# Kernel tuning notes

Hardware: AMD Instinct MI355X
Metric: run time of the kernel (lower is better)

## Reference

```python
import jax, jax.numpy as jnp
import numpy as np

MARGIN = 1.0  # cur_margin for LBA_inverted_loss=True
COS_SCALE = 128.0


def smoothed_metric_loss(X, margin=MARGIN):
    # X: [B, E]. Lifted structured loss with inverted cosine similarity.
    B = X.shape[0]
    P = B // 2
    D = (X @ X.T) / COS_SCALE            # [B, B]
    E = jnp.exp(margin + D)              # [B, B]
    # For pair p (rows i=2p, j=2p+1): sum E over rows {i,j}, all columns except {i,j}.
    Eb = E.reshape(P, 2, P, 2)           # [P, 2, P, 2]
    row_sums = Eb.sum(axis=(1, 2, 3))    # [P] full sum over both rows of pair p
    idx = jnp.arange(P)
    diag_block = Eb[idx, :, idx, :].sum(axis=(1, 2))  # [P] the excluded 2x2 block
    S = row_sums - diag_block            # [P] masked sums
    Dij = D.reshape(P, 2, P, 2)[idx, 0, idx, 1]       # [P] D[i, j]
    J = jnp.log(S) - Dij
    return 0.5 * jnp.mean(J * J)


def reference(text_embeddings, shape_embeddings):
    B = text_embeddings.shape[0]
    # shape_embeddings repeated twice per model: row k -> shape[k // 2]
    shape_rep = jnp.repeat(shape_embeddings, 2, axis=0)      # [B, E]
    metric_tt = smoothed_metric_loss(text_embeddings)
    # mask rows: even rows keep text, odd rows take repeated shape embedding
    even = (jnp.arange(B) % 2 == 0)[:, None]
    mixed = jnp.where(even, text_embeddings, shape_rep)      # [B, E]
    metric_st = smoothed_metric_loss(mixed)
    return metric_tt + metric_st


def setup_inputs() -> dict:
    key = jax.random.key(0)
    k1, k2 = jax.random.split(key)
    B, E = 8192, 128
    text_embeddings = jax.random.normal(k1, (B, E), dtype=jnp.float32)
    shape_embeddings = jax.random.normal(k2, (B // 2, E), dtype=jnp.float32)
    return {"text_embeddings": text_embeddings, "shape_embeddings": shape_embeddings}
```

## Files before the change

kernel.cpp:

```cpp
#include <hip/hip_runtime.h>
#include <hip/hip_bf16.h>


#define B_ROWS 8192
#define E_COLS 128
#define P_PAIRS 4096
#define NSTRIP 128
#define NH 8

using f32x4 = __attribute__((ext_vector_type(4))) float;
using i32x8 = __attribute__((ext_vector_type(8))) int;

#define BF_SCALE 0.106164482742544f
#define EULER    2.718281828459045f
#define SCALE1   0x7f

__device__ __forceinline__ unsigned pk4_fp8(float a, float b, float c, float d) {
    unsigned v = 0;
    v = __builtin_amdgcn_cvt_pk_fp8_f32(a * BF_SCALE, b * BF_SCALE, v, false);
    v = __builtin_amdgcn_cvt_pk_fp8_f32(c * BF_SCALE, d * BF_SCALE, v, true);
    return v;
}

__device__ __forceinline__ int lds_off(int row, int k0) {
    return (row << 7) + (k0 ^ ((row & 7) << 4));
}

__device__ __forceinline__ i32x8 load_frag32(const char* base, int row, int k32) {
    union { i32x8 v; int4 h[2]; } u;
    u.h[0] = *(const int4*)(base + lds_off(row, k32));
    u.h[1] = *(const int4*)(base + lds_off(row, k32 + 16));
    return u.v;
}

__device__ __forceinline__ void stage8k(const char* gsrc, char* ldst, int tid) {
#pragma unroll
    for (int it = 0; it < 2; ++it) {
        int L   = it * 4096 + tid * 16;
        int row = L >> 7;
        int cb  = L & 127;
        int src = (row << 7) + (cb ^ ((row & 7) << 4));
        __builtin_amdgcn_global_load_lds(
            (const __attribute__((address_space(1))) void*)(gsrc + src),
            (__attribute__((address_space(3))) void*)(ldst + L), 16, 0, 0);
    }
}

__global__ void convert_kernel(const float* __restrict__ text,
                               const float* __restrict__ shape,
                               unsigned* __restrict__ Xt,
                               unsigned* __restrict__ Xm,
                               float* __restrict__ R,
                               float* __restrict__ out) {
    int idx = blockIdx.x * blockDim.x + threadIdx.x;
    if (idx >= B_ROWS * E_COLS / 4) return;
    if (idx < 4096) {
        float4 z; z.x = z.y = z.z = z.w = 0.f;
        ((float4*)R)[idx] = z;
    }
    if (idx == 0) *out = 0.f;
    int e = idx * 4;
    float4 t = *(const float4*)(text + e);
    unsigned tp = pk4_fp8(t.x, t.y, t.z, t.w);
    Xt[idx] = tp;
    int row = e >> 7;
    if (row & 1) {
        int col = e & 127;
        float4 s = *(const float4*)(shape + (row >> 1) * E_COLS + col);
        Xm[idx] = pk4_fp8(s.x, s.y, s.z, s.w);
    } else {
        Xm[idx] = tp;
    }
}

__launch_bounds__(256, 8)
__global__ void gemm_rowsum_kernel(const unsigned char* __restrict__ Xt,
                                   const unsigned char* __restrict__ Xm,
                                   float* __restrict__ R) {
    const int bm = blockIdx.x, h = blockIdx.y, l = blockIdx.z;
    const char* gX = (const char*)(l ? Xm : Xt);

    __shared__ __align__(16) char buf0[64 * 128];
    __shared__ __align__(16) char buf1[64 * 128];
    const int tid = threadIdx.x;

    const int t0 = (h == 0) ? NH : h;
    const int N  = (h == 0) ? (bm < 64 ? 8 : 7) : 8;

    stage8k(gX + (size_t)bm * 8192, buf0, tid);
    stage8k(gX + (size_t)((bm + t0) & 127) * 8192, buf1, tid);
    asm volatile("s_waitcnt vmcnt(2)" ::: "memory");
    __builtin_amdgcn_s_barrier();

    const int lane = tid & 63;
    const int w  = tid >> 6;
    const int wr = w >> 1, wc = w & 1;
    const int rA0 = wr * 32 + (lane & 15);
    const int rB0 = wc * 32 + (lane & 15);
    const int k32 = (lane >> 4) * 32;

    i32x8 afr[2];
#pragma unroll
    for (int m = 0; m < 2; ++m)
        afr[m] = load_frag32(buf0, rA0 + m * 16, k32);

    float s_r[2][4] = {{0.f}};

    if (h == 0) {
        i32x8 bfr[2];
#pragma unroll
        for (int n = 0; n < 2; ++n)
            bfr[n] = load_frag32(buf0, rB0 + n * 16, k32);
        f32x4 acc[2][2] = {};
#pragma unroll
        for (int m = 0; m < 2; ++m)
#pragma unroll
            for (int n = 0; n < 2; ++n)
                acc[m][n] = __builtin_amdgcn_mfma_scale_f32_16x16x128_f8f6f4(
                    afr[m], bfr[n], acc[m][n], 0, 0, 0, SCALE1, 0, SCALE1);
#pragma unroll
        for (int m = 0; m < 2; ++m)
#pragma unroll
            for (int n = 0; n < 2; ++n)
#pragma unroll
                for (int j = 0; j < 4; ++j)
                    s_r[m][j] += __builtin_amdgcn_exp2f(acc[m][n][j]);
    }

    asm volatile("s_waitcnt lgkmcnt(0)" ::: "memory");
    __builtin_amdgcn_s_barrier();

    int cur = 1;
    for (int idx = 0; idx < N; ++idx) {
        const bool hasnext = (idx + 1 < N);
        if (hasnext)
            stage8k(gX + (size_t)((bm + t0 + NH * (idx + 1)) & 127) * 8192,
                    cur ? buf0 : buf1, tid);

        if (hasnext) { asm volatile("s_waitcnt vmcnt(2)" ::: "memory"); }
        else         { asm volatile("s_waitcnt vmcnt(0)" ::: "memory"); }
        __builtin_amdgcn_s_barrier();

        const char* lsrc = cur ? buf1 : buf0;
        i32x8 bfr[2];
#pragma unroll
        for (int n = 0; n < 2; ++n)
            bfr[n] = load_frag32(lsrc, rB0 + n * 16, k32);
        f32x4 acc[2][2] = {};
#pragma unroll
        for (int m = 0; m < 2; ++m)
#pragma unroll
            for (int n = 0; n < 2; ++n)
                acc[m][n] = __builtin_amdgcn_mfma_scale_f32_16x16x128_f8f6f4(
                    afr[m], bfr[n], acc[m][n], 0, 0, 0, SCALE1, 0, SCALE1);

        asm volatile("s_waitcnt lgkmcnt(0)" ::: "memory");
        __builtin_amdgcn_s_barrier();

        const int bn = (bm + t0 + NH * idx) & 127;
        float s_c[2] = {0.f, 0.f};
#pragma unroll
        for (int m = 0; m < 2; ++m)
#pragma unroll
            for (int n = 0; n < 2; ++n)
#pragma unroll
                for (int j = 0; j < 4; ++j) {
                    float e2 = __builtin_amdgcn_exp2f(acc[m][n][j]);
                    s_r[m][j] += e2;
                    s_c[n] += e2;
                }
#pragma unroll
        for (int n = 0; n < 2; ++n) {
            float v = s_c[n];
            v += __shfl_xor(v, 16, 64);
            v += __shfl_xor(v, 32, 64);
            if (lane < 16) {
                int gcol = bn * 64 + wc * 32 + n * 16 + lane;
                atomicAdd(&R[l * B_ROWS + gcol], EULER * v);
            }
        }
        cur ^= 1;
    }

#pragma unroll
    for (int m = 0; m < 2; ++m)
#pragma unroll
        for (int j = 0; j < 4; ++j) {
            float v = s_r[m][j];
            v += __shfl_xor(v, 1, 64);
            v += __shfl_xor(v, 2, 64);
            v += __shfl_xor(v, 4, 64);
            v += __shfl_xor(v, 8, 64);
            if ((lane & 15) == 0) {
                int grow = bm * 64 + wr * 32 + m * 16 + (lane >> 4) * 4 + j;
                atomicAdd(&R[l * B_ROWS + grow], EULER * v);
            }
        }
}

__global__ void finalize_kernel(const float* __restrict__ text,
                                const float* __restrict__ shape,
                                const float* __restrict__ R,
                                float* __restrict__ out) {
    const int tid = threadIdx.x;
    const int lane = tid & 63;
    const int w = tid >> 6;
    const float inv128 = 0.0078125f;
    float accum = 0.f;

    for (int task = blockIdx.x * 4 + w; task < 2 * P_PAIRS; task += 1024) {
        int l = task >> 12;
        int p = task & (P_PAIRS - 1);
        const float* a = text + (2 * p) * E_COLS;
        const float* b = l ? (shape + p * E_COLS) : (text + (2 * p + 1) * E_COLS);
        float2 av = *(const float2*)(a + lane * 2);
        float2 bv = *(const float2*)(b + lane * 2);
        float dii = av.x * av.x + av.y * av.y;
        float djj = bv.x * bv.x + bv.y * bv.y;
        float dij = av.x * bv.x + av.y * bv.y;
#pragma unroll
        for (int sh = 1; sh < 64; sh <<= 1) {
            dii += __shfl_xor(dii, sh, 64);
            djj += __shfl_xor(djj, sh, 64);
            dij += __shfl_xor(dij, sh, 64);
        }
        if (lane == 0) {
            float Dii = dii * inv128, Djj = djj * inv128, Dij = dij * inv128;
            float S = R[l * B_ROWS + 2 * p] + R[l * B_ROWS + 2 * p + 1]
                    - (__expf(1.f + Dii) + 2.f * __expf(1.f + Dij) + __expf(1.f + Djj));
            float J = __logf(S) - Dij;
            accum += 0.5f * J * J * (1.0f / (float)P_PAIRS);
        }
    }

    __shared__ float red[4];
    if (lane == 0) red[w] = accum;
    __syncthreads();
    if (tid == 0) atomicAdd(out, red[0] + red[1] + red[2] + red[3]);
}

extern "C" void kernel_launch(void* const* d_in, const int* in_sizes, int n_in,
                              void* d_out, int out_size, void* d_ws, size_t ws_size,
                              hipStream_t stream) {
    const float* text  = (const float*)d_in[0];
    const float* shape = (const float*)d_in[1];
    float* out = (float*)d_out;
    char* ws = (char*)d_ws;

    unsigned char* Xt = (unsigned char*)ws;
    unsigned char* Xm = (unsigned char*)(ws + 1u * 1024u * 1024u);
    float* R = (float*)(ws + 2u * 1024u * 1024u);

    convert_kernel<<<(B_ROWS * E_COLS / 4 + 255) / 256, 256, 0, stream>>>(
        text, shape, (unsigned*)Xt, (unsigned*)Xm, R, out);

    dim3 grid(NSTRIP, NH, 2);
    gemm_rowsum_kernel<<<grid, 256, 0, stream>>>(Xt, Xm, R);

    finalize_kernel<<<256, 256, 0, stream>>>(text, shape, R, out);
}
```

Baseline: 48.25 us.

## Restructure GEMM tile per-wave with private triple-buffered LDS and no barriers

Each wave now owns all 64 A rows (loaded directly from global into registers) and a private 16-row slice of B, staged into its own triple-buffered LDS region. This removes the block-wide barriers and shared double buffer. The loop is fully unrolled over 8 tiles, and the h==0 case's extra tile is masked by multiplying by zero instead of running a variable trip count. MFMA sections get raised priority, and launch bounds drop to 5 blocks per SM to make room for the larger register footprint. The masked tile still spends its exp and atomic work.

```diff
diff --git a/kernel.cpp b/kernel.cpp
--- a/kernel.cpp
+++ b/kernel.cpp
@@ -22,28 +22,11 @@
     return v;
 }
 
-__device__ __forceinline__ int lds_off(int row, int k0) {
-    return (row << 7) + (k0 ^ ((row & 7) << 4));
-}
-
-__device__ __forceinline__ i32x8 load_frag32(const char* base, int row, int k32) {
+__device__ __forceinline__ i32x8 load_frag32_g(const char* rowbase, int k32) {
     union { i32x8 v; int4 h[2]; } u;
-    u.h[0] = *(const int4*)(base + lds_off(row, k32));
-    u.h[1] = *(const int4*)(base + lds_off(row, k32 + 16));
+    u.h[0] = *(const int4*)(rowbase + k32);
+    u.h[1] = *(const int4*)(rowbase + k32 + 16);
     return u.v;
-}
-
-__device__ __forceinline__ void stage8k(const char* gsrc, char* ldst, int tid) {
-#pragma unroll
-    for (int it = 0; it < 2; ++it) {
-        int L   = it * 4096 + tid * 16;
-        int row = L >> 7;
-        int cb  = L & 127;
-        int src = (row << 7) + (cb ^ ((row & 7) << 4));
-        __builtin_amdgcn_global_load_lds(
-            (const __attribute__((address_space(1))) void*)(gsrc + src),
-            (__attribute__((address_space(3))) void*)(ldst + L), 16, 0, 0);
-    }
 }
 
 __global__ void convert_kernel(const float* __restrict__ text,
@@ -73,117 +56,113 @@
     }
 }
 
-__launch_bounds__(256, 8)
+__launch_bounds__(256, 5)
 __global__ void gemm_rowsum_kernel(const unsigned char* __restrict__ Xt,
                                    const unsigned char* __restrict__ Xm,
                                    float* __restrict__ R) {
     const int bm = blockIdx.x, h = blockIdx.y, l = blockIdx.z;
     const char* gX = (const char*)(l ? Xm : Xt);
 
-    __shared__ __align__(16) char buf0[64 * 128];
-    __shared__ __align__(16) char buf1[64 * 128];
-    const int tid = threadIdx.x;
+    __shared__ __align__(16) char lds[4][3][16 * 128];
+    const int tid  = threadIdx.x;
+    const int lane = tid & 63;
+    const int w    = tid >> 6;
 
     const int t0 = (h == 0) ? NH : h;
-    const int N  = (h == 0) ? (bm < 64 ? 8 : 7) : 8;
-
-    stage8k(gX + (size_t)bm * 8192, buf0, tid);
-    stage8k(gX + (size_t)((bm + t0) & 127) * 8192, buf1, tid);
-    asm volatile("s_waitcnt vmcnt(2)" ::: "memory");
-    __builtin_amdgcn_s_barrier();
-
-    const int lane = tid & 63;
-    const int w  = tid >> 6;
-    const int wr = w >> 1, wc = w & 1;
-    const int rA0 = wr * 32 + (lane & 15);
-    const int rB0 = wc * 32 + (lane & 15);
-    const int k32 = (lane >> 4) * 32;
-
-    i32x8 afr[2];
-#pragma unroll
-    for (int m = 0; m < 2; ++m)
-        afr[m] = load_frag32(buf0, rA0 + m * 16, k32);
-
-    float s_r[2][4] = {{0.f}};
+    const float g7 = (h == 0 && bm >= 64) ? 0.f : 1.f;
+
+    const int lrow = lane & 15;
+    const int kb   = (lane >> 4) * 32;
+
+    auto stage = [&](int bn, char* dst) {
+        const char* base = gX + (size_t)bn * 8192 + w * (16 * 128);
+#pragma unroll
+        for (int it = 0; it < 2; ++it) {
+            int sr  = it * 8 + (lane >> 3);
+            int cb  = (lane & 7) * 16;
+            int src = sr * 128 + (cb ^ ((sr & 7) << 4));
+            __builtin_amdgcn_global_load_lds(
+                (const __attribute__((address_space(1))) void*)(base + src),
+                (__attribute__((address_space(3))) void*)(dst + it * 1024), 16, 0, 0);
+        }
+    };
+    auto ldfrag = [&](const char* regn) {
+        union { i32x8 v; int4 h2[2]; } u;
+        u.h2[0] = *(const int4*)(regn + lrow * 128 + (kb        ^ ((lrow & 7) << 4)));
+        u.h2[1] = *(const int4*)(regn + lrow * 128 + ((kb + 16) ^ ((lrow & 7) << 4)));
+        return u.v;
+    };
+    auto bn_of = [&](int k) { return (bm + t0 + 8 * k) & 127; };
+
+    const char* Ag = gX + (size_t)bm * 8192;
+    i32x8 afr[4];
+#pragma unroll
+    for (int m = 0; m < 4; ++m)
+        afr[m] = load_frag32_g(Ag + (size_t)(m * 16 + lrow) * 128, kb);
+
+    i32x8 db = {};
+    if (h == 0)
+        db = load_frag32_g(Ag + (size_t)(w * 16 + lrow) * 128, kb);
+
+    stage(bn_of(0), &lds[w][0][0]);
+    stage(bn_of(1), &lds[w][1][0]);
+
+    asm volatile("s_waitcnt vmcnt(4)" ::: "memory");
+
+    float s_r[4][4] = {{0.f}};
 
     if (h == 0) {
-        i32x8 bfr[2];
-#pragma unroll
-        for (int n = 0; n < 2; ++n)
-            bfr[n] = load_frag32(buf0, rB0 + n * 16, k32);
-        f32x4 acc[2][2] = {};
-#pragma unroll
-        for (int m = 0; m < 2; ++m)
-#pragma unroll
-            for (int n = 0; n < 2; ++n)
-                acc[m][n] = __builtin_amdgcn_mfma_scale_f32_16x16x128_f8f6f4(
-                    afr[m], bfr[n], acc[m][n], 0, 0, 0, SCALE1, 0, SCALE1);
-#pragma unroll
-        for (int m = 0; m < 2; ++m)
-#pragma unroll
-            for (int n = 0; n < 2; ++n)
-#pragma unroll
-                for (int j = 0; j < 4; ++j)
-                    s_r[m][j] += __builtin_amdgcn_exp2f(acc[m][n][j]);
-    }
-
-    asm volatile("s_waitcnt lgkmcnt(0)" ::: "memory");
-    __builtin_amdgcn_s_barrier();
-
-    int cur = 1;
-    for (int idx = 0; idx < N; ++idx) {
-        const bool hasnext = (idx + 1 < N);
-        if (hasnext)
-            stage8k(gX + (size_t)((bm + t0 + NH * (idx + 1)) & 127) * 8192,
-                    cur ? buf0 : buf1, tid);
-
-        if (hasnext) { asm volatile("s_waitcnt vmcnt(2)" ::: "memory"); }
-        else         { asm volatile("s_waitcnt vmcnt(0)" ::: "memory"); }
-        __builtin_amdgcn_s_barrier();
-
-        const char* lsrc = cur ? buf1 : buf0;
-        i32x8 bfr[2];
-#pragma unroll
-        for (int n = 0; n < 2; ++n)
-            bfr[n] = load_frag32(lsrc, rB0 + n * 16, k32);
-        f32x4 acc[2][2] = {};
-#pragma unroll
-        for (int m = 0; m < 2; ++m)
-#pragma unroll
-            for (int n = 0; n < 2; ++n)
-                acc[m][n] = __builtin_amdgcn_mfma_scale_f32_16x16x128_f8f6f4(
-                    afr[m], bfr[n], acc[m][n], 0, 0, 0, SCALE1, 0, SCALE1);
-
-        asm volatile("s_waitcnt lgkmcnt(0)" ::: "memory");
-        __builtin_amdgcn_s_barrier();
-
-        const int bn = (bm + t0 + NH * idx) & 127;
-        float s_c[2] = {0.f, 0.f};
-#pragma unroll
-        for (int m = 0; m < 2; ++m)
-#pragma unroll
-            for (int n = 0; n < 2; ++n)
-#pragma unroll
-                for (int j = 0; j < 4; ++j) {
-                    float e2 = __builtin_amdgcn_exp2f(acc[m][n][j]);
-                    s_r[m][j] += e2;
-                    s_c[n] += e2;
-                }
-#pragma unroll
-        for (int n = 0; n < 2; ++n) {
-            float v = s_c[n];
-            v += __shfl_xor(v, 16, 64);
-            v += __shfl_xor(v, 32, 64);
-            if (lane < 16) {
-                int gcol = bn * 64 + wc * 32 + n * 16 + lane;
-                atomicAdd(&R[l * B_ROWS + gcol], EULER * v);
+        f32x4 acc[4] = {};
+#pragma unroll
+        for (int m = 0; m < 4; ++m)
+            acc[m] = __builtin_amdgcn_mfma_scale_f32_16x16x128_f8f6f4(
+                afr[m], db, acc[m], 0, 0, 0, SCALE1, 0, SCALE1);
+#pragma unroll
+        for (int m = 0; m < 4; ++m)
+#pragma unroll
+            for (int j = 0; j < 4; ++j)
+                s_r[m][j] += __builtin_amdgcn_exp2f(acc[m][j]);
+    }
+
+#pragma unroll
+    for (int k = 0; k < 8; ++k) {
+        if (k + 2 < 8)
+            stage(bn_of(k + 2), &lds[w][(k + 2) % 3][0]);
+
+        if (k + 2 < 8)      { asm volatile("s_waitcnt vmcnt(4)" ::: "memory"); }
+        else if (k + 1 < 8) { asm volatile("s_waitcnt vmcnt(2)" ::: "memory"); }
+        else                { asm volatile("s_waitcnt vmcnt(0)" ::: "memory"); }
+
+        i32x8 bfr = ldfrag(&lds[w][k % 3][0]);
+
+        f32x4 acc[4] = {};
+        __builtin_amdgcn_s_setprio(1);
+#pragma unroll
+        for (int m = 0; m < 4; ++m)
+            acc[m] = __builtin_amdgcn_mfma_scale_f32_16x16x128_f8f6f4(
+                afr[m], bfr, acc[m], 0, 0, 0, SCALE1, 0, SCALE1);
+        __builtin_amdgcn_s_setprio(0);
+
+        const float g = (k == 7) ? g7 : 1.f;
+        float sc = 0.f;
+#pragma unroll
+        for (int m = 0; m < 4; ++m)
+#pragma unroll
+            for (int j = 0; j < 4; ++j) {
+                float e2 = __builtin_amdgcn_exp2f(acc[m][j]) * g;
+                s_r[m][j] += e2;
+                sc += e2;
             }
-        }
-        cur ^= 1;
-    }
-
-#pragma unroll
-    for (int m = 0; m < 2; ++m)
+        sc += __shfl_xor(sc, 16, 64);
+        sc += __shfl_xor(sc, 32, 64);
+        if (lane < 16) {
+            int gcol = bn_of(k) * 64 + w * 16 + lane;
+            atomicAdd(&R[l * B_ROWS + gcol], EULER * sc);
+        }
+    }
+
+#pragma unroll
+    for (int m = 0; m < 4; ++m)
 #pragma unroll
         for (int j = 0; j < 4; ++j) {
             float v = s_r[m][j];
@@ -192,7 +171,7 @@
             v += __shfl_xor(v, 4, 64);
             v += __shfl_xor(v, 8, 64);
             if ((lane & 15) == 0) {
-                int grow = bm * 64 + wr * 32 + m * 16 + (lane >> 4) * 4 + j;
+                int grow = bm * 64 + m * 16 + (lane >> 4) * 4 + j;
                 atomicAdd(&R[l * B_ROWS + grow], EULER * v);
             }
         }
```

Measured after the change: 104.3 us. +116.2%, slower.
